# Kernel tuning notes

Hardware: AMD Instinct MI355X
Metric: run time of the kernel (lower is better)

Reference implementation:

```python
import math
import jax, jax.numpy as jnp
import numpy as np

B, S, D, E, K, H = 4, 1024, 768, 8, 2, 2048
NH_ROUTER, NH_COLLAB = 12, 2  # collab heads = min(n_heads, top_k) = 2
EPS = 1e-5


def setup_inputs() -> dict:
    key = jax.random.key(0)
    ks = jax.random.split(key, 16)
    n = lambda k, shp, s=0.02: jax.random.normal(k, shp, jnp.float32) * s
    return {
        "x": jax.random.normal(ks[0], (B, S, D), jnp.float32),
        # parallel expert params (E, D, H) / (E, H, D)
        "w1": n(ks[1], (E, D, H)), "w3": n(ks[2], (E, D, H)), "w2": n(ks[3], (E, H, D)),
        # router self-attention (torch MultiheadAttention packed qkv + out proj)
        "r_in_w": n(ks[4], (3 * D, D)), "r_in_b": jnp.zeros((3 * D,), jnp.float32),
        "r_out_w": n(ks[5], (D, D)), "r_out_b": jnp.zeros((D,), jnp.float32),
        "r_norm_w": jnp.ones((D,), jnp.float32),
        "gate_w": n(ks[6], (E, D)),
        # collaborative cross-attention
        "c_in_w": n(ks[7], (3 * D, D)), "c_in_b": jnp.zeros((3 * D,), jnp.float32),
        "c_out_w": n(ks[8], (D, D)), "c_out_b": jnp.zeros((D,), jnp.float32),
        "c_norm_w": jnp.ones((D,), jnp.float32),
        "ffn_w1": n(ks[9], (D, D)), "ffn_w2": n(ks[10], (D, D)),
        "o_w": n(ks[11], (D, D)),
    }


def _mha(x, in_w, in_b, out_w, out_b, nh):
    # torch nn.MultiheadAttention, batch_first, q=k=v=x; returns out and head-avg probs
    N, L, Dm = x.shape
    hd = Dm // nh
    qkv = x @ in_w.T + in_b                       # (N, L, 3D)
    q, k, v = jnp.split(qkv, 3, axis=-1)
    sp = lambda t: t.reshape(N, L, nh, hd).transpose(0, 2, 1, 3)
    q, k, v = sp(q), sp(k), sp(v)
    probs = jax.nn.softmax(jnp.einsum('nhld,nhmd->nhlm', q, k) / math.sqrt(hd), axis=-1)
    o = jnp.einsum('nhlm,nhmd->nhld', probs, v).transpose(0, 2, 1, 3).reshape(N, L, Dm)
    return o @ out_w.T + out_b, probs.mean(axis=1)


def _rms(x, w):
    return x * jax.lax.rsqrt(jnp.mean(x * x, axis=-1, keepdims=True) + EPS) * w


def reference(x, w1, w3, w2, r_in_w, r_in_b, r_out_w, r_out_b, r_norm_w, gate_w,
              c_in_w, c_in_b, c_out_w, c_out_b, c_norm_w, ffn_w1, ffn_w2, o_w):
    Bx, Sx, Dx = x.shape
    # dense all-expert SwiGLU: (B,S,E,D)
    gate = jnp.einsum('bsd,edh->bseh', x, w1)
    up = jnp.einsum('bsd,edh->bseh', x, w3)
    expert_out = jnp.einsum('bseh,ehd->bsed', jax.nn.silu(gate) * up, w2)
    ef = expert_out.reshape(Bx * Sx, E, Dx)
    # attention-based router over the E experts per token
    ctx, _ = _mha(ef, r_in_w, r_in_b, r_out_w, r_out_b, NH_ROUTER)
    ctx = _rms(ctx + ef, r_norm_w)
    logits = (ctx.mean(axis=1) @ gate_w.T).reshape(Bx, Sx, E)
    routing_probs = jax.nn.softmax(logits, axis=-1)
    tk_logits, tk_idx = jax.lax.top_k(logits, K)  # router_temperature = 1.0
    tk_probs = jax.nn.softmax(tk_logits, axis=-1)
    sel = jnp.take_along_axis(expert_out, tk_idx[..., None], axis=2)  # (B,S,K,D)
    sf = sel.reshape(Bx * Sx, K, Dx)
    # collaborative fusion among selected experts
    ao, aw = _mha(sf, c_in_w, c_in_b, c_out_w, c_out_b, NH_COLLAB)
    ao = _rms(ao + sf, c_norm_w)
    refined = (jax.nn.gelu(ao @ ffn_w1.T, approximate=False) @ ffn_w2.T) + ao
    refined = refined.reshape(Bx, Sx, K, Dx)
    final = jnp.sum(refined * tk_probs[..., None], axis=2) @ o_w.T
    # auxiliary loss
    usage = routing_probs.mean(axis=(0, 1))
    balance = jnp.mean((usage - usage.mean()) ** 2)
    diversity = jnp.mean(-jnp.sum(aw * jnp.log(aw + 1e-9), axis=-1))
    aux = 0.1 * (0.01 * diversity + 0.01 * balance)
    return final, aux, tk_idx
```

## Files before the change

### kernel.cpp

```cpp
#include <hip/hip_runtime.h>


typedef unsigned short u16;
typedef unsigned int u32;
typedef _Float16 f16;
typedef f16 f16x4 __attribute__((ext_vector_type(4)));
typedef f16 f16x8 __attribute__((ext_vector_type(8)));
typedef float f32x4 __attribute__((ext_vector_type(4)));

__device__ __forceinline__ float b2f(u16 v){
  union { u32 u; float f; } x; x.u = ((u32)v) << 16; return x.f;
}
__device__ __forceinline__ u16 f2b(float f){
  union { float f; u32 u; } x; x.f = f;
  u32 u = x.u;
  if ((u & 0x7fffffffu) > 0x7f800000u) return (u16)0x7fc0;
  return (u16)((u + 0x7fffu + ((u >> 16) & 1u)) >> 16);
}
__device__ __forceinline__ float gelu_f(float x){
  return 0.5f * x * (1.f + erff(x * 0.70710678118654752f));
}

template<int NW>
__device__ __forceinline__ float blockReduceSum(float v, float* red){
  #pragma unroll
  for (int o = 32; o > 0; o >>= 1) v += __shfl_down(v, o, 64);
  const int wv = threadIdx.x >> 6, ln = threadIdx.x & 63;
  __syncthreads();
  if (ln == 0) red[wv] = v;
  __syncthreads();
  float s = 0.f;
  #pragma unroll
  for (int i = 0; i < NW; i++) s += red[i];
  return s;
}

__device__ __forceinline__ float waveReduceSum(float v){
  #pragma unroll
  for (int o = 32; o > 0; o >>= 1) v += __shfl_xor(v, o, 64);
  return v;
}

template<int AK, int AOP, bool SPLIT, bool BT, bool BIAS, int ACT, bool RES, bool DUAL, bool SK2>
__global__ __launch_bounds__(256, 2) void mgemm(
    const void* __restrict__ Ap, const float* __restrict__ A2p, int lda, long long strideA,
    const float* __restrict__ B1, const float* __restrict__ B2, int ldb, long long strideB,
    float* __restrict__ C1, float* __restrict__ C2, int ldc, long long strideC,
    const float* __restrict__ bias, const float* __restrict__ resid, int ldr,
    int Kd, int zs)
{
  __shared__ f16 AsH[2][128*40];
  __shared__ f16 BsH[2][128*40];
  __shared__ f16 AsL[SPLIT ? 2 : 1][SPLIT ? 128*40 : 4];
  __shared__ f16 BsL[SPLIT ? 2 : 1][SPLIT ? 128*40 : 4];

  const int tid = threadIdx.x;
  const int m0 = blockIdx.y * 128, n0 = blockIdx.x * 128;
  const int z = blockIdx.z;
  int zi = z, k0 = 0, KL = Kd;
  const float* Bz; float* Cz;
  if constexpr (DUAL){
    if (z < zs){ zi = z;      Bz = B1 + (long long)zi*strideB; Cz = C1 + (long long)zi*strideC; }
    else       { zi = z - zs; Bz = B2 + (long long)zi*strideB; Cz = C2 + (long long)zi*strideC; }
  } else if constexpr (SK2){
    const int s = (z >= zs) ? 1 : 0;
    zi = z - s * zs;
    KL = Kd >> 1; k0 = s * KL;
    Bz = B1 + (long long)zi*strideB + (BT ? (long long)k0 : (long long)k0 * ldb);
    Cz = (s ? C2 : C1) + (long long)zi*strideC;
  } else {
    Bz = B1 + (long long)z*strideB; Cz = C1 + (long long)z*strideC;
  }
  const float* A32  = (const float*)Ap + (AK==0 ? (long long)zi*strideA : 0) + k0;
  const u16*   A16  = (const u16*)Ap   + (AK==1 ? (long long)zi*strideA : 0) + k0;
  const float* A32b = (AOP != 0) ? (A2p + (long long)zi*strideA + k0) : nullptr;

  const int ln = tid & 63, wv = tid >> 6;
  const int wm = (wv >> 1) * 64, wn = (wv & 1) * 64;
  const int fr = ln & 15, fq = ln >> 4;

  const int rA = tid >> 1, kcA = (tid & 1) * 16;
  const int npB = tid & 63, kgB = tid >> 6;

  struct Regs {
    f32x4 av[4]; f32x4 av2[4]; uint4 av16[2]; f32x4 bv[4]; float2 bw[8];
  };
  Regs R0, R1;

  auto loadAB = [&](Regs& R, int kt){
    if constexpr (AK == 0){
      const float* s = A32 + (size_t)(m0 + rA) * lda + kt + kcA;
      #pragma unroll
      for (int j = 0; j < 4; j++) R.av[j] = ((const f32x4*)s)[j];
      if constexpr (AOP != 0){
        const float* s2 = A32b + (size_t)(m0 + rA) * lda + kt + kcA;
        #pragma unroll
        for (int j = 0; j < 4; j++) R.av2[j] = ((const f32x4*)s2)[j];
      }
    } else {
      const u16* s = A16 + (size_t)(m0 + rA) * lda + kt + kcA;
      R.av16[0] = ((const uint4*)s)[0]; R.av16[1] = ((const uint4*)s)[1];
    }
    if constexpr (BT){
      const float* s = Bz + (size_t)(n0 + rA) * ldb + kt + kcA;
      #pragma unroll
      for (int j = 0; j < 4; j++) R.bv[j] = ((const f32x4*)s)[j];
    } else {
      const float* s = Bz + (size_t)(kt + kgB * 8) * ldb + n0 + 2 * npB;
      #pragma unroll
      for (int kk = 0; kk < 8; kk++) R.bw[kk] = *(const float2*)(s + (size_t)kk * ldb);
    }
  };

  auto storeAB = [&](const Regs& R, int b){
    if constexpr (AK == 0){
      #pragma unroll
      for (int jj = 0; jj < 2; jj++){
        f16x8 h, l;
        #pragma unroll
        for (int c = 0; c < 8; c++){
          float v = R.av[jj*2 + (c>>2)][c & 3];
          if constexpr (AOP == 1){
            const float u = R.av2[jj*2 + (c>>2)][c & 3];
            v = (v / (1.f + expf(-v))) * u;
          } else if constexpr (AOP == 2){
            v = v + R.av2[jj*2 + (c>>2)][c & 3];
          } else if constexpr (AOP == 3){
            v = gelu_f(v + R.av2[jj*2 + (c>>2)][c & 3]);
          }
          h[c] = (f16)v;
          if constexpr (SPLIT) l[c] = (f16)(v - (float)h[c]);
        }
        *(f16x8*)&AsH[b][rA*40 + kcA + jj*8] = h;
        if constexpr (SPLIT) *(f16x8*)&AsL[b][rA*40 + kcA + jj*8] = l;
      }
    } else {
      #pragma unroll
      for (int j = 0; j < 2; j++){
        const uint4 v = R.av16[j];
        f16x8 h;
        h[0]=(f16)b2f((u16)(v.x & 0xffff)); h[1]=(f16)b2f((u16)(v.x >> 16));
        h[2]=(f16)b2f((u16)(v.y & 0xffff)); h[3]=(f16)b2f((u16)(v.y >> 16));
        h[4]=(f16)b2f((u16)(v.z & 0xffff)); h[5]=(f16)b2f((u16)(v.z >> 16));
        h[6]=(f16)b2f((u16)(v.w & 0xffff)); h[7]=(f16)b2f((u16)(v.w >> 16));
        *(f16x8*)&AsH[b][rA*40 + kcA + j*8] = h;
      }
    }
    if constexpr (BT){
      #pragma unroll
      for (int jj = 0; jj < 2; jj++){
        f16x8 h, l;
        #pragma unroll
        for (int c = 0; c < 8; c++){
          const float v = R.bv[jj*2 + (c>>2)][c & 3];
          h[c] = (f16)v;
          if constexpr (SPLIT) l[c] = (f16)(v - (float)h[c]);
        }
        *(f16x8*)&BsH[b][rA*40 + kcA + jj*8] = h;
        if constexpr (SPLIT) *(f16x8*)&BsL[b][rA*40 + kcA + jj*8] = l;
      }
    } else {
      #pragma unroll
      for (int c = 0; c < 2; c++){
        const int row = 2*npB + c;
        const int p8 = (kgB + (row >> 3)) & 3;
        f16x8 h, l;
        #pragma unroll
        for (int kk = 0; kk < 8; kk++){
          const float v = c ? R.bw[kk].y : R.bw[kk].x;
          h[kk] = (f16)v;
          if constexpr (SPLIT) l[kk] = (f16)(v - (float)h[kk]);
        }
        *(f16x8*)&BsH[b][row*40 + p8*8] = h;
        if constexpr (SPLIT) *(f16x8*)&BsL[b][row*40 + p8*8] = l;
      }
    }
  };

  f32x4 acc[4][4];
  #pragma unroll
  for (int i = 0; i < 4; i++)
    #pragma unroll
    for (int j = 0; j < 4; j++){ acc[i][j][0]=0.f; acc[i][j][1]=0.f; acc[i][j][2]=0.f; acc[i][j][3]=0.f; }

  int aoff[4], boff[4];
  #pragma unroll
  for (int i = 0; i < 4; i++) aoff[i] = (wm + i*16 + fr)*40 + fq*8;
  #pragma unroll
  for (int j = 0; j < 4; j++){
    const int brow = wn + j*16 + fr;
    boff[j] = brow*40 + (BT ? fq*8 : (((fq + (brow >> 3)) & 3) << 3));
  }

  auto compute = [&](int b){
    f16x8 aH[4], bH[4];
    #pragma unroll
    for (int i = 0; i < 4; i++) aH[i] = *(const f16x8*)&AsH[b][aoff[i]];
    #pragma unroll
    for (int j = 0; j < 4; j++) bH[j] = *(const f16x8*)&BsH[b][boff[j]];
    #pragma unroll
    for (int i = 0; i < 4; i++)
      #pragma unroll
      for (int j = 0; j < 4; j++)
        acc[i][j] = __builtin_amdgcn_mfma_f32_16x16x32_f16(aH[i], bH[j], acc[i][j], 0, 0, 0);
    if constexpr (SPLIT){
      f16x8 aL[4], bL[4];
      #pragma unroll
      for (int i = 0; i < 4; i++) aL[i] = *(const f16x8*)&AsL[b][aoff[i]];
      #pragma unroll
      for (int j = 0; j < 4; j++) bL[j] = *(const f16x8*)&BsL[b][boff[j]];
      #pragma unroll
      for (int i = 0; i < 4; i++)
        #pragma unroll
        for (int j = 0; j < 4; j++){
          acc[i][j] = __builtin_amdgcn_mfma_f32_16x16x32_f16(aH[i], bL[j], acc[i][j], 0, 0, 0);
          acc[i][j] = __builtin_amdgcn_mfma_f32_16x16x32_f16(aL[i], bH[j], acc[i][j], 0, 0, 0);
        }
    }
  };

  const int NT = KL >> 5;
  loadAB(R0, 0);
  loadAB(R1, 32);
  for (int tt = 0; tt < NT; tt += 2){
    storeAB(R0, 0);
    __syncthreads();
    if (tt + 2 < NT) loadAB(R0, (tt + 2) << 5);
    compute(0);
    storeAB(R1, 1);
    __syncthreads();
    if (tt + 3 < NT) loadAB(R1, (tt + 3) << 5);
    compute(1);
  }

  #pragma unroll
  for (int j = 0; j < 4; j++){
    const int n = n0 + wn + j*16 + fr;
    float bvv = 0.f;
    if constexpr (BIAS) bvv = bias[n];
    #pragma unroll
    for (int i = 0; i < 4; i++){
      #pragma unroll
      for (int r = 0; r < 4; r++){
        const int m = m0 + wm + i*16 + fq*4 + r;
        float v = acc[i][j][r];
        if constexpr (BIAS) v += bvv;
        if constexpr (ACT == 1) v = gelu_f(v);
        if constexpr (RES) v += resid[(size_t)m * ldr + n];
        Cz[(size_t)m * ldc + n] = v;
      }
    }
  }
}

__global__ void silu_k(const float4* __restrict__ g, const float4* __restrict__ u,
                       float4* __restrict__ h, int n4){
  const int i = blockIdx.x * 256 + threadIdx.x;
  if (i < n4){
    const float4 gv = g[i], uv = u[i];
    float4 r;
    r.x = (gv.x / (1.f + expf(-gv.x))) * uv.x;
    r.y = (gv.y / (1.f + expf(-gv.y))) * uv.y;
    r.z = (gv.z / (1.f + expf(-gv.z))) * uv.z;
    r.w = (gv.w / (1.f + expf(-gv.w))) * uv.w;
    h[i] = r;
  }
}

template<int ACT, bool RES, bool BIAS>
__global__ void add2_k(float* __restrict__ dst, const float* __restrict__ src,
                       const float* __restrict__ bias, const float* __restrict__ resid,
                       int n4, int ld4){
  const int i = blockIdx.x * 256 + threadIdx.x;
  if (i >= n4) return;
  const f32x4 a = ((const f32x4*)dst)[i];
  const f32x4 b = ((const f32x4*)src)[i];
  const int c4 = (i % ld4) * 4;
  f32x4 r;
  #pragma unroll
  for (int c = 0; c < 4; c++){
    float v = a[c] + b[c];
    if constexpr (BIAS) v += bias[c4 + c];
    if constexpr (ACT == 1) v = gelu_f(v);
    if constexpr (RES) v += resid[(size_t)i * 4 + c];
    r[c] = v;
  }
  ((f32x4*)dst)[i] = r;
}

__global__ __launch_bounds__(128) void router_attn(const float* __restrict__ qkv,
                                                   float* __restrict__ attn_o){
  __shared__ __align__(16) float L[8 * 1536];
  __shared__ float Ps[96][8];
  const int t = blockIdx.x, tid = threadIdx.x;
  const float* src = qkv + (size_t)t * 8 * 2304;
  for (int i = tid; i < 3072; i += 128){
    const int e = i / 384, c4 = i - e * 384;
    ((float4*)L)[i] = ((const float4*)(src + (size_t)e * 2304))[c4];
  }
  __syncthreads();
  if (tid < 96){
    const int h = tid >> 3, e = tid & 7;
    const float* q = L + e * 1536 + h * 64;
    float s[8]; float mx = -1e30f;
    #pragma unroll
    for (int e2 = 0; e2 < 8; e2++){
      const float* kk = L + e2 * 1536 + 768 + h * 64;
      float acc = 0.f;
      #pragma unroll
      for (int d = 0; d < 64; d++) acc = fmaf(q[d], kk[d], acc);
      s[e2] = acc * 0.125f;
      mx = fmaxf(mx, s[e2]);
    }
    float den = 0.f;
    #pragma unroll
    for (int e2 = 0; e2 < 8; e2++){ s[e2] = expf(s[e2] - mx); den += s[e2]; }
    const float inv = 1.f / den;
    #pragma unroll
    for (int e2 = 0; e2 < 8; e2++) Ps[tid][e2] = s[e2] * inv;
  }
  __syncthreads();
  for (int i = tid; i < 1536; i += 128){
    const int e = i / 192, c4 = i - e * 192;
    ((float4*)L)[i] = ((const float4*)(src + (size_t)e * 2304 + 1536))[c4];
  }
  __syncthreads();
  if (tid < 96){
    const int h = tid >> 3, e = tid & 7;
    float p[8];
    #pragma unroll
    for (int e2 = 0; e2 < 8; e2++) p[e2] = Ps[tid][e2];
    float* dst = attn_o + ((size_t)t * 8 + e) * 768 + h * 64;
    for (int d = 0; d < 64; d++){
      float acc = 0.f;
      #pragma unroll
      for (int e2 = 0; e2 < 8; e2++) acc = fmaf(p[e2], L[e2 * 768 + h * 64 + d], acc);
      dst[d] = acc;
    }
  }
}

__global__ __launch_bounds__(256) void router_final(
    const float* __restrict__ proj0, const float* __restrict__ proj1,
    const float* __restrict__ pbias, const float* __restrict__ eoc,
    const float* __restrict__ rnw, const float* __restrict__ gw,
    int t0, float* __restrict__ usage, float* __restrict__ tkp,
    u16* __restrict__ sf, float* __restrict__ oidx)
{
  const int wv = threadIdx.x >> 6, ln = threadIdx.x & 63;
  const int tl = blockIdx.x * 4 + wv, t = t0 + tl;

  float rw[12], pb[12];
  #pragma unroll
  for (int g = 0; g < 3; g++){
    const f32x4 w = ((const f32x4*)rnw)[ln + g * 64];
    const f32x4 bbv = ((const f32x4*)pbias)[ln + g * 64];
    #pragma unroll
    for (int c = 0; c < 4; c++){ rw[g*4 + c] = w[c]; pb[g*4 + c] = bbv[c]; }
  }

  float cs[12];
  #pragma unroll
  for (int i = 0; i < 12; i++) cs[i] = 0.f;

  for (int e = 0; e < 8; e++){
    const size_t ro = ((size_t)tl * 8 + e) * 768;
    float v[12]; float ss = 0.f;
    #pragma unroll
    for (int g = 0; g < 3; g++){
      const f32x4 p0 = ((const f32x4*)(proj0 + ro))[ln + g * 64];
      const f32x4 p1 = ((const f32x4*)(proj1 + ro))[ln + g * 64];
      const f32x4 e0 = ((const f32x4*)(eoc + ro))[ln + g * 64];
      #pragma unroll
      for (int c = 0; c < 4; c++){
        const float vv = ((p0[c] + p1[c]) + pb[g*4 + c]) + e0[c];
        v[g*4 + c] = vv; ss += vv * vv;
      }
    }
    ss = waveReduceSum(ss);
    const float sc = 1.f / sqrtf(ss * (1.f / 768.f) + 1e-5f);
    #pragma unroll
    for (int i = 0; i < 12; i++) cs[i] += v[i] * sc * rw[i];
  }

  float lg[8];
  #pragma unroll
  for (int j = 0; j < 8; j++){
    const float* gwr = gw + j * 768;
    float p = 0.f;
    #pragma unroll
    for (int g = 0; g < 3; g++){
      const f32x4 w = ((const f32x4*)gwr)[ln + g * 64];
      #pragma unroll
      for (int c = 0; c < 4; c++) p += cs[g*4 + c] * w[c];
    }
    lg[j] = waveReduceSum(p) * 0.125f;
  }

  int i0 = 0; float l0 = lg[0];
  #pragma unroll
  for (int j = 1; j < 8; j++) if (lg[j] > l0){ l0 = lg[j]; i0 = j; }
  int i1 = -1; float l1 = -1e30f;
  #pragma unroll
  for (int j = 0; j < 8; j++) if (j != i0 && lg[j] > l1){ l1 = lg[j]; i1 = j; }

  if (ln == 0){
    float mx = -1e30f;
    #pragma unroll
    for (int j = 0; j < 8; j++) mx = fmaxf(mx, lg[j]);
    float ex[8], den = 0.f;
    #pragma unroll
    for (int j = 0; j < 8; j++){ ex[j] = expf(lg[j] - mx); den += ex[j]; }
    const float inv = 1.f / den;
    #pragma unroll
    for (int j = 0; j < 8; j++) atomicAdd(&usage[j], ex[j] * inv);
    const float e1v = expf(l1 - l0);
    const float p0 = 1.f / (1.f + e1v);
    tkp[(size_t)t * 2]     = p0;
    tkp[(size_t)t * 2 + 1] = e1v * p0;
    oidx[(size_t)t * 2]     = (float)i0;
    oidx[(size_t)t * 2 + 1] = (float)i1;
  }

  #pragma unroll
  for (int s = 0; s < 2; s++){
    const int ie = s ? i1 : i0;
    const size_t ro = ((size_t)tl * 8 + ie) * 768;
    #pragma unroll
    for (int g = 0; g < 3; g++){
      const f32x4 a = ((const f32x4*)(eoc + ro))[ln + g * 64];
      ushort4 o;
      o.x = f2b(a[0]); o.y = f2b(a[1]); o.z = f2b(a[2]); o.w = f2b(a[3]);
      *(ushort4*)&sf[((size_t)t * 2 + s) * 768 + 4 * (ln + g * 64)] = o;
    }
  }
}

__global__ __launch_bounds__(128) void collab_attn(
    const float* __restrict__ qkv, float* __restrict__ attn_o, float* __restrict__ divsum)
{
  const int t = blockIdx.x, tid = threadIdx.x;
  __shared__ __align__(16) float L[4608];
  __shared__ float P[8];
  __shared__ float red[2];
  const float* src = qkv + (size_t)t * 4608;
  for (int i = tid; i < 1152; i += 128) ((float4*)L)[i] = ((const float4*)src)[i];
  __syncthreads();
  for (int hij = 0; hij < 8; hij++){
    const int h = hij >> 2, qi = (hij >> 1) & 1, kj = hij & 1;
    const float* q = L + qi * 2304 + h * 384;
    const float* k = L + kj * 2304 + 768 + h * 384;
    float acc = 0.f;
    for (int d = tid; d < 384; d += 128) acc += q[d] * k[d];
    acc = blockReduceSum<2>(acc, red);
    if (tid == 0) P[hij] = acc;
  }
  __syncthreads();
  if (tid == 0){
    const float scale = 0.051031036307982884f;
    float aw[2][2] = {{0.f,0.f},{0.f,0.f}};
    for (int h = 0; h < 2; h++)
      for (int i = 0; i < 2; i++){
        const float s0 = P[h*4 + i*2 + 0] * scale, s1 = P[h*4 + i*2 + 1] * scale;
        const float m = fmaxf(s0, s1);
        const float e0 = expf(s0 - m), e1 = expf(s1 - m), inv = 1.f / (e0 + e1);
        P[h*4 + i*2 + 0] = e0 * inv; P[h*4 + i*2 + 1] = e1 * inv;
        aw[i][0] += 0.5f * e0 * inv; aw[i][1] += 0.5f * e1 * inv;
      }
    float ent = 0.f;
    for (int i = 0; i < 2; i++)
      for (int j = 0; j < 2; j++) ent -= aw[i][j] * logf(aw[i][j] + 1e-9f);
    atomicAdd(divsum, ent);
  }
  __syncthreads();
  for (int c = tid; c < 768; c += 128){
    const int h = c / 384;
    const float v0 = L[1536 + c], v1 = L[3840 + c];
    attn_o[((size_t)t * 2 + 0) * 768 + c] = P[h*4 + 0] * v0 + P[h*4 + 1] * v1;
    attn_o[((size_t)t * 2 + 1) * 768 + c] = P[h*4 + 2] * v0 + P[h*4 + 3] * v1;
  }
}

__global__ __launch_bounds__(256) void rms2_k(
    const float* __restrict__ a0, const float* __restrict__ a1,
    const float* __restrict__ bb, const u16* __restrict__ rb,
    const float* __restrict__ wt, float* __restrict__ o){
  const int r = blockIdx.x, tid = threadIdx.x;
  __shared__ float red[4];
  float v[3]; float ss = 0.f;
  #pragma unroll
  for (int i = 0; i < 3; i++){
    const int c = tid + i * 256;
    const float t = (a0[(size_t)r * 768 + c] + a1[(size_t)r * 768 + c]) + bb[c];
    v[i] = t + b2f(rb[(size_t)r * 768 + c]);
    ss += v[i] * v[i];
  }
  ss = blockReduceSum<4>(ss, red);
  const float sc = 1.f / sqrtf(ss * (1.f / 768.f) + 1e-5f);
  #pragma unroll
  for (int i = 0; i < 3; i++){
    const int c = tid + i * 256;
    o[(size_t)r * 768 + c] = v[i] * sc * wt[c];
  }
}

__global__ void wsum3(const float* __restrict__ pA, const float* __restrict__ pB,
                      const float* __restrict__ ao, const float* __restrict__ tkp,
                      float* __restrict__ y){
  const int idx = blockIdx.x * 256 + threadIdx.x;
  const int t = idx / 768, c = idx - t * 768;
  const size_t r0 = ((size_t)t * 2) * 768 + c, r1 = r0 + 768;
  const float v0 = (pA[r0] + pB[r0]) + ao[r0];
  const float v1 = (pA[r1] + pB[r1]) + ao[r1];
  y[idx] = tkp[t * 2] * v0 + tkp[t * 2 + 1] * v1;
}

__global__ void aux_k(const float* __restrict__ usage, const float* __restrict__ divsum,
                      float* __restrict__ out){
  if (threadIdx.x == 0 && blockIdx.x == 0){
    float u[8], s = 0.f;
    for (int e = 0; e < 8; e++){ u[e] = usage[e] * (1.f / 4096.f); s += u[e]; }
    const float mean = s * 0.125f;
    float bal = 0.f;
    for (int e = 0; e < 8; e++){ const float d = u[e] - mean; bal += d * d; }
    bal *= 0.125f;
    const float div = divsum[0] * (1.f / 8192.f);
    out[0] = 0.1f * (0.01f * div + 0.01f * bal);
  }
}

__global__ void zero_k(float* p, int n){
  const int i = blockIdx.x * 64 + threadIdx.x;
  if (i < n) p[i] = 0.f;
}

extern "C" void kernel_launch(void* const* d_in, const int* in_sizes, int n_in,
                              void* d_out, int out_size, void* d_ws, size_t ws_size,
                              hipStream_t stream)
{
  (void)in_sizes; (void)n_in; (void)out_size; (void)ws_size;
  const float* x       = (const float*)d_in[0];
  const float* w1      = (const float*)d_in[1];
  const float* w3      = (const float*)d_in[2];
  const float* w2      = (const float*)d_in[3];
  const float* r_in_w  = (const float*)d_in[4];
  const float* r_in_b  = (const float*)d_in[5];
  const float* r_out_w = (const float*)d_in[6];
  const float* r_out_b = (const float*)d_in[7];
  const float* r_norm_w= (const float*)d_in[8];
  const float* gate_w  = (const float*)d_in[9];
  const float* c_in_w  = (const float*)d_in[10];
  const float* c_in_b  = (const float*)d_in[11];
  const float* c_out_w = (const float*)d_in[12];
  const float* c_out_b = (const float*)d_in[13];
  const float* c_norm_w= (const float*)d_in[14];
  const float* ffn_w1  = (const float*)d_in[15];
  const float* ffn_w2  = (const float*)d_in[16];
  const float* o_w     = (const float*)d_in[17];

  char* wsb   = (char*)d_ws;
  char* arena = wsb;
  float* eoc  = (float*)(wsb + 33554432);
  u16*   sf   = (u16*)  (wsb + 39845888);
  float* tkp  = (float*)(wsb + 52428800);
  float* usage= (float*)(wsb + 52461568);

  float* gateb = (float*)(arena);
  float* upb   = (float*)(arena + 16777216);
  float* qkvr  = (float*)(arena);
  float* aor   = (float*)(arena + 18874368);
  float* projr = (float*)(arena + 25165824);
  float* pr2   = (float*)(arena);

  float* qkvc  = (float*)(arena);
  float* aoc   = (float*)(arena + 18874368);
  float* pc1   = (float*)(arena + 25165824);
  float* pc2   = (float*)(arena);
  float* aob   = (float*)(arena + 6291456);
  float* pf1   = (float*)(arena + 12582912);
  float* pf2   = (float*)(arena + 18874368);
  float* ybuf  = (float*)(arena + 12582912);
  float* fo2   = (float*)(arena + 18874368);

  float* outp    = (float*)d_out;
  float* out_aux = outp + (size_t)4096*768;
  float* out_idx = out_aux + 1;

  zero_k<<<1, 64, 0, stream>>>(usage, 16);

  for (int cch = 0; cch < 16; cch++){
    const int t0 = cch * 256;
    mgemm<0,0,true,false,false,0,false,true,false><<<dim3(16,2,16),256,0,stream>>>(
      x + (size_t)t0*768, nullptr, 768, 0LL,
      w1, w3, 2048, 1572864LL,
      gateb, upb, 2048, 524288LL,
      nullptr, nullptr, 0, 768, 8);
    silu_k<<<4096, 256, 0, stream>>>((const float4*)gateb, (const float4*)upb,
                                     (float4*)gateb, 1048576);
    mgemm<0,0,true,false,false,0,false,false,true><<<dim3(6,2,16),256,0,stream>>>(
      gateb, nullptr, 2048, 524288LL,
      w2, nullptr, 768, 1572864LL,
      eoc, upb, 6144, 768LL,
      nullptr, nullptr, 0, 2048, 8);
    add2_k<0,false,false><<<1536, 256, 0, stream>>>(eoc, upb, nullptr, nullptr, 393216, 192);
    mgemm<0,0,true,true,true,0,false,false,false><<<dim3(18,16,1),256,0,stream>>>(
      eoc, nullptr, 768, 0LL, r_in_w, nullptr, 768, 0LL,
      qkvr, nullptr, 2304, 0LL, r_in_b, nullptr, 0, 768, 0);
    router_attn<<<256, 128, 0, stream>>>(qkvr, aor);
    mgemm<0,0,true,true,false,0,false,false,true><<<dim3(6,16,2),256,0,stream>>>(
      aor, nullptr, 768, 0LL, r_out_w, nullptr, 768, 0LL,
      projr, pr2, 768, 0LL, nullptr, nullptr, 0, 768, 1);
    router_final<<<64, 256, 0, stream>>>(projr, pr2, r_out_b, eoc,
                                         r_norm_w, gate_w, t0, usage, tkp, sf, out_idx);
  }

  for (int q = 0; q < 4; q++){
    const int tq0 = q * 1024;
    const u16* sf_q = sf + (size_t)tq0 * 2 * 768;
    mgemm<1,0,false,true,true,0,false,false,false><<<dim3(18,16,1),256,0,stream>>>(
      sf_q, nullptr, 768, 0LL, c_in_w, nullptr, 768, 0LL,
      qkvc, nullptr, 2304, 0LL, c_in_b, nullptr, 0, 768, 0);
    collab_attn<<<1024, 128, 0, stream>>>(qkvc, aoc, usage + 8);
    mgemm<0,0,false,true,false,0,false,false,true><<<dim3(6,16,2),256,0,stream>>>(
      aoc, nullptr, 768, 0LL, c_out_w, nullptr, 768, 0LL,
      pc1, pc2, 768, 0LL, nullptr, nullptr, 0, 768, 1);
    rms2_k<<<2048, 256, 0, stream>>>(pc1, pc2, c_out_b, sf_q, c_norm_w, aob);
    mgemm<0,0,false,true,false,0,false,false,true><<<dim3(6,16,2),256,0,stream>>>(
      aob, nullptr, 768, 0LL, ffn_w1, nullptr, 768, 0LL,
      pf1, pf2, 768, 0LL, nullptr, nullptr, 0, 768, 1);
    mgemm<0,3,false,true,false,0,false,false,true><<<dim3(6,16,2),256,0,stream>>>(
      pf1, pf2, 768, 0LL, ffn_w2, nullptr, 768, 0LL,
      pc1, pc2, 768, 0LL, nullptr, nullptr, 0, 768, 1);
    wsum3<<<3072, 256, 0, stream>>>(pc1, pc2, aob, tkp + (size_t)tq0 * 2, ybuf);
    mgemm<0,0,false,true,false,0,false,false,true><<<dim3(6,8,2),256,0,stream>>>(
      ybuf, nullptr, 768, 0LL, o_w, nullptr, 768, 0LL,
      outp + (size_t)tq0 * 768, fo2, 768, 0LL, nullptr, nullptr, 0, 768, 1);
    add2_k<0,false,false><<<768, 256, 0, stream>>>(outp + (size_t)tq0 * 768, fo2,
                                                   nullptr, nullptr, 196608, 192);
  }
  aux_k<<<1, 64, 0, stream>>>(usage, usage + 8, out_aux);
}
```

Before: 4.444 ms.

## Use nontemporal loads/stores for streaming intermediates and simplify GEMM prefetch to single register set

Adds an NTC template flag so GEMM epilogues write results with nontemporal stores, and switches the elementwise, attention and reduction kernels to nontemporal loads and stores on intermediate buffers that are read once. This aims to keep the large streamed intermediates from evicting reused weights in cache. The GEMM main loop also drops the two-register-set prefetch for a single set loaded one tile ahead, and unused AOP fusion branches are removed. This lowers register pressure but shortens the prefetch distance, and nontemporal stores can hurt when the next kernel rereads the data right away.

```diff
diff --git a/kernel.cpp b/kernel.cpp
--- a/kernel.cpp
+++ b/kernel.cpp
@@ -41,7 +41,7 @@
   return v;
 }
 
-template<int AK, int AOP, bool SPLIT, bool BT, bool BIAS, int ACT, bool RES, bool DUAL, bool SK2>
+template<int AK, int AOP, bool SPLIT, bool BT, bool BIAS, int ACT, bool RES, bool DUAL, bool SK2, bool NTC>
 __global__ __launch_bounds__(256, 2) void mgemm(
     const void* __restrict__ Ap, const float* __restrict__ A2p, int lda, long long strideA,
     const float* __restrict__ B1, const float* __restrict__ B2, int ldb, long long strideB,
@@ -82,51 +82,43 @@
   const int rA = tid >> 1, kcA = (tid & 1) * 16;
   const int npB = tid & 63, kgB = tid >> 6;
 
-  struct Regs {
-    f32x4 av[4]; f32x4 av2[4]; uint4 av16[2]; f32x4 bv[4]; float2 bw[8];
-  };
-  Regs R0, R1;
-
-  auto loadAB = [&](Regs& R, int kt){
+  f32x4 av[4]; f32x4 av2[4]; uint4 av16[2]; f32x4 bv[4]; float2 bw[8];
+
+  auto loadAB = [&](int kt){
     if constexpr (AK == 0){
       const float* s = A32 + (size_t)(m0 + rA) * lda + kt + kcA;
       #pragma unroll
-      for (int j = 0; j < 4; j++) R.av[j] = ((const f32x4*)s)[j];
+      for (int j = 0; j < 4; j++) av[j] = ((const f32x4*)s)[j];
       if constexpr (AOP != 0){
         const float* s2 = A32b + (size_t)(m0 + rA) * lda + kt + kcA;
         #pragma unroll
-        for (int j = 0; j < 4; j++) R.av2[j] = ((const f32x4*)s2)[j];
+        for (int j = 0; j < 4; j++) av2[j] = ((const f32x4*)s2)[j];
       }
     } else {
       const u16* s = A16 + (size_t)(m0 + rA) * lda + kt + kcA;
-      R.av16[0] = ((const uint4*)s)[0]; R.av16[1] = ((const uint4*)s)[1];
+      av16[0] = ((const uint4*)s)[0]; av16[1] = ((const uint4*)s)[1];
     }
     if constexpr (BT){
       const float* s = Bz + (size_t)(n0 + rA) * ldb + kt + kcA;
       #pragma unroll
-      for (int j = 0; j < 4; j++) R.bv[j] = ((const f32x4*)s)[j];
+      for (int j = 0; j < 4; j++) bv[j] = ((const f32x4*)s)[j];
     } else {
       const float* s = Bz + (size_t)(kt + kgB * 8) * ldb + n0 + 2 * npB;
       #pragma unroll
-      for (int kk = 0; kk < 8; kk++) R.bw[kk] = *(const float2*)(s + (size_t)kk * ldb);
+      for (int kk = 0; kk < 8; kk++) bw[kk] = *(const float2*)(s + (size_t)kk * ldb);
     }
   };
 
-  auto storeAB = [&](const Regs& R, int b){
+  auto storeAB = [&](int b){
     if constexpr (AK == 0){
       #pragma unroll
       for (int jj = 0; jj < 2; jj++){
         f16x8 h, l;
         #pragma unroll
         for (int c = 0; c < 8; c++){
-          float v = R.av[jj*2 + (c>>2)][c & 3];
-          if constexpr (AOP == 1){
-            const float u = R.av2[jj*2 + (c>>2)][c & 3];
-            v = (v / (1.f + expf(-v))) * u;
-          } else if constexpr (AOP == 2){
-            v = v + R.av2[jj*2 + (c>>2)][c & 3];
-          } else if constexpr (AOP == 3){
-            v = gelu_f(v + R.av2[jj*2 + (c>>2)][c & 3]);
+          float v = av[jj*2 + (c>>2)][c & 3];
+          if constexpr (AOP == 3){
+            v = gelu_f(v + av2[jj*2 + (c>>2)][c & 3]);
           }
           h[c] = (f16)v;
           if constexpr (SPLIT) l[c] = (f16)(v - (float)h[c]);
@@ -137,7 +129,7 @@
     } else {
       #pragma unroll
       for (int j = 0; j < 2; j++){
-        const uint4 v = R.av16[j];
+        const uint4 v = av16[j];
         f16x8 h;
         h[0]=(f16)b2f((u16)(v.x & 0xffff)); h[1]=(f16)b2f((u16)(v.x >> 16));
         h[2]=(f16)b2f((u16)(v.y & 0xffff)); h[3]=(f16)b2f((u16)(v.y >> 16));
@@ -152,7 +144,7 @@
         f16x8 h, l;
         #pragma unroll
         for (int c = 0; c < 8; c++){
-          const float v = R.bv[jj*2 + (c>>2)][c & 3];
+          const float v = bv[jj*2 + (c>>2)][c & 3];
           h[c] = (f16)v;
           if constexpr (SPLIT) l[c] = (f16)(v - (float)h[c]);
         }
@@ -167,7 +159,7 @@
         f16x8 h, l;
         #pragma unroll
         for (int kk = 0; kk < 8; kk++){
-          const float v = c ? R.bw[kk].y : R.bw[kk].x;
+          const float v = c ? bw[kk].y : bw[kk].x;
           h[kk] = (f16)v;
           if constexpr (SPLIT) l[kk] = (f16)(v - (float)h[kk]);
         }
@@ -192,7 +184,13 @@
     boff[j] = brow*40 + (BT ? fq*8 : (((fq + (brow >> 3)) & 3) << 3));
   }
 
-  auto compute = [&](int b){
+  loadAB(0);
+  const int NT = KL >> 5;
+  for (int t = 0; t < NT; t++){
+    const int b = t & 1;
+    storeAB(b);
+    __syncthreads();
+    if (t + 1 < NT) loadAB((t + 1) << 5);
     f16x8 aH[4], bH[4];
     #pragma unroll
     for (int i = 0; i < 4; i++) aH[i] = *(const f16x8*)&AsH[b][aoff[i]];
@@ -217,20 +215,6 @@
           acc[i][j] = __builtin_amdgcn_mfma_f32_16x16x32_f16(aL[i], bH[j], acc[i][j], 0, 0, 0);
         }
     }
-  };
-
-  const int NT = KL >> 5;
-  loadAB(R0, 0);
-  loadAB(R1, 32);
-  for (int tt = 0; tt < NT; tt += 2){
-    storeAB(R0, 0);
-    __syncthreads();
-    if (tt + 2 < NT) loadAB(R0, (tt + 2) << 5);
-    compute(0);
-    storeAB(R1, 1);
-    __syncthreads();
-    if (tt + 3 < NT) loadAB(R1, (tt + 3) << 5);
-    compute(1);
   }
 
   #pragma unroll
@@ -247,23 +231,24 @@
         if constexpr (BIAS) v += bvv;
         if constexpr (ACT == 1) v = gelu_f(v);
         if constexpr (RES) v += resid[(size_t)m * ldr + n];
-        Cz[(size_t)m * ldc + n] = v;
-      }
-    }
-  }
-}
-
-__global__ void silu_k(const float4* __restrict__ g, const float4* __restrict__ u,
-                       float4* __restrict__ h, int n4){
+        if constexpr (NTC) __builtin_nontemporal_store(v, &Cz[(size_t)m * ldc + n]);
+        else               Cz[(size_t)m * ldc + n] = v;
+      }
+    }
+  }
+}
+
+__global__ void silu_k(const f32x4* __restrict__ g, const f32x4* __restrict__ u,
+                       f32x4* __restrict__ h, int n4){
   const int i = blockIdx.x * 256 + threadIdx.x;
   if (i < n4){
-    const float4 gv = g[i], uv = u[i];
-    float4 r;
-    r.x = (gv.x / (1.f + expf(-gv.x))) * uv.x;
-    r.y = (gv.y / (1.f + expf(-gv.y))) * uv.y;
-    r.z = (gv.z / (1.f + expf(-gv.z))) * uv.z;
-    r.w = (gv.w / (1.f + expf(-gv.w))) * uv.w;
-    h[i] = r;
+    const f32x4 gv = __builtin_nontemporal_load(&g[i]);
+    const f32x4 uv = __builtin_nontemporal_load(&u[i]);
+    f32x4 r;
+    #pragma unroll
+    for (int c = 0; c < 4; c++)
+      r[c] = (gv[c] / (1.f + expf(-gv[c]))) * uv[c];
+    __builtin_nontemporal_store(r, &h[i]);
   }
 }
 
@@ -273,8 +258,8 @@
                        int n4, int ld4){
   const int i = blockIdx.x * 256 + threadIdx.x;
   if (i >= n4) return;
-  const f32x4 a = ((const f32x4*)dst)[i];
-  const f32x4 b = ((const f32x4*)src)[i];
+  const f32x4 a = __builtin_nontemporal_load(&((const f32x4*)dst)[i]);
+  const f32x4 b = __builtin_nontemporal_load(&((const f32x4*)src)[i]);
   const int c4 = (i % ld4) * 4;
   f32x4 r;
   #pragma unroll
@@ -285,7 +270,7 @@
     if constexpr (RES) v += resid[(size_t)i * 4 + c];
     r[c] = v;
   }
-  ((f32x4*)dst)[i] = r;
+  __builtin_nontemporal_store(r, &((f32x4*)dst)[i]);
 }
 
 __global__ __launch_bounds__(128) void router_attn(const float* __restrict__ qkv,
@@ -296,7 +281,7 @@
   const float* src = qkv + (size_t)t * 8 * 2304;
   for (int i = tid; i < 3072; i += 128){
     const int e = i / 384, c4 = i - e * 384;
-    ((float4*)L)[i] = ((const float4*)(src + (size_t)e * 2304))[c4];
+    ((f32x4*)L)[i] = __builtin_nontemporal_load(&((const f32x4*)(src + (size_t)e * 2304))[c4]);
   }
   __syncthreads();
   if (tid < 96){
@@ -322,7 +307,7 @@
   __syncthreads();
   for (int i = tid; i < 1536; i += 128){
     const int e = i / 192, c4 = i - e * 192;
-    ((float4*)L)[i] = ((const float4*)(src + (size_t)e * 2304 + 1536))[c4];
+    ((f32x4*)L)[i] = __builtin_nontemporal_load(&((const f32x4*)(src + (size_t)e * 2304 + 1536))[c4]);
   }
   __syncthreads();
   if (tid < 96){
@@ -368,8 +353,8 @@
     float v[12]; float ss = 0.f;
     #pragma unroll
     for (int g = 0; g < 3; g++){
-      const f32x4 p0 = ((const f32x4*)(proj0 + ro))[ln + g * 64];
-      const f32x4 p1 = ((const f32x4*)(proj1 + ro))[ln + g * 64];
+      const f32x4 p0 = __builtin_nontemporal_load(&((const f32x4*)(proj0 + ro))[ln + g * 64]);
+      const f32x4 p1 = __builtin_nontemporal_load(&((const f32x4*)(proj1 + ro))[ln + g * 64]);
       const f32x4 e0 = ((const f32x4*)(eoc + ro))[ln + g * 64];
       #pragma unroll
       for (int c = 0; c < 4; c++){
@@ -444,7 +429,8 @@
   __shared__ float P[8];
   __shared__ float red[2];
   const float* src = qkv + (size_t)t * 4608;
-  for (int i = tid; i < 1152; i += 128) ((float4*)L)[i] = ((const float4*)src)[i];
+  for (int i = tid; i < 1152; i += 128)
+    ((f32x4*)L)[i] = __builtin_nontemporal_load(&((const f32x4*)src)[i]);
   __syncthreads();
   for (int hij = 0; hij < 8; hij++){
     const int h = hij >> 2, qi = (hij >> 1) & 1, kj = hij & 1;
@@ -491,7 +477,8 @@
   #pragma unroll
   for (int i = 0; i < 3; i++){
     const int c = tid + i * 256;
-    const float t = (a0[(size_t)r * 768 + c] + a1[(size_t)r * 768 + c]) + bb[c];
+    const float t = (__builtin_nontemporal_load(&a0[(size_t)r * 768 + c])
+                   + __builtin_nontemporal_load(&a1[(size_t)r * 768 + c])) + bb[c];
     v[i] = t + b2f(rb[(size_t)r * 768 + c]);
     ss += v[i] * v[i];
   }
@@ -510,8 +497,8 @@
   const int idx = blockIdx.x * 256 + threadIdx.x;
   const int t = idx / 768, c = idx - t * 768;
   const size_t r0 = ((size_t)t * 2) * 768 + c, r1 = r0 + 768;
-  const float v0 = (pA[r0] + pB[r0]) + ao[r0];
-  const float v1 = (pA[r1] + pB[r1]) + ao[r1];
+  const float v0 = (__builtin_nontemporal_load(&pA[r0]) + __builtin_nontemporal_load(&pB[r0])) + ao[r0];
+  const float v1 = (__builtin_nontemporal_load(&pA[r1]) + __builtin_nontemporal_load(&pB[r1])) + ao[r1];
   y[idx] = tkp[t * 2] * v0 + tkp[t * 2 + 1] * v1;
 }
 
@@ -590,24 +577,24 @@
 
   for (int cch = 0; cch < 16; cch++){
     const int t0 = cch * 256;
-    mgemm<0,0,true,false,false,0,false,true,false><<<dim3(16,2,16),256,0,stream>>>(
+    mgemm<0,0,true,false,false,0,false,true,false,true><<<dim3(16,2,16),256,0,stream>>>(
       x + (size_t)t0*768, nullptr, 768, 0LL,
       w1, w3, 2048, 1572864LL,
       gateb, upb, 2048, 524288LL,
       nullptr, nullptr, 0, 768, 8);
-    silu_k<<<4096, 256, 0, stream>>>((const float4*)gateb, (const float4*)upb,
-                                     (float4*)gateb, 1048576);
-    mgemm<0,0,true,false,false,0,false,false,true><<<dim3(6,2,16),256,0,stream>>>(
+    silu_k<<<4096, 256, 0, stream>>>((const f32x4*)gateb, (const f32x4*)upb,
+                                     (f32x4*)gateb, 1048576);
+    mgemm<0,0,true,false,false,0,false,false,true,true><<<dim3(6,2,16),256,0,stream>>>(
       gateb, nullptr, 2048, 524288LL,
       w2, nullptr, 768, 1572864LL,
       eoc, upb, 6144, 768LL,
       nullptr, nullptr, 0, 2048, 8);
     add2_k<0,false,false><<<1536, 256, 0, stream>>>(eoc, upb, nullptr, nullptr, 393216, 192);
-    mgemm<0,0,true,true,true,0,false,false,false><<<dim3(18,16,1),256,0,stream>>>(
+    mgemm<0,0,true,true,true,0,false,false,false,true><<<dim3(18,16,1),256,0,stream>>>(
       eoc, nullptr, 768, 0LL, r_in_w, nullptr, 768, 0LL,
       qkvr, nullptr, 2304, 0LL, r_in_b, nullptr, 0, 768, 0);
     router_attn<<<256, 128, 0, stream>>>(qkvr, aor);
-    mgemm<0,0,true,true,false,0,false,false,true><<<dim3(6,16,2),256,0,stream>>>(
+    mgemm<0,0,true,true,false,0,false,false,true,true><<<dim3(6,16,2),256,0,stream>>>(
       aor, nullptr, 768, 0LL, r_out_w, nullptr, 768, 0LL,
       projr, pr2, 768, 0LL, nullptr, nullptr, 0, 768, 1);
     router_final<<<64, 256, 0, stream>>>(projr, pr2, r_out_b, eoc,
@@ -617,22 +604,22 @@
   for (int q = 0; q < 4; q++){
     const int tq0 = q * 1024;
     const u16* sf_q = sf + (size_t)tq0 * 2 * 768;
-    mgemm<1,0,false,true,true,0,false,false,false><<<dim3(18,16,1),256,0,stream>>>(
+    mgemm<1,0,false,true,true,0,false,false,false,true><<<dim3(18,16,1),256,0,stream>>>(
       sf_q, nullptr, 768, 0LL, c_in_w, nullptr, 768, 0LL,
       qkvc, nullptr, 2304, 0LL, c_in_b, nullptr, 0, 768, 0);
     collab_attn<<<1024, 128, 0, stream>>>(qkvc, aoc, usage + 8);
-    mgemm<0,0,false,true,false,0,false,false,true><<<dim3(6,16,2),256,0,stream>>>(
+    mgemm<0,0,false,true,false,0,false,false,true,true><<<dim3(6,16,2),256,0,stream>>>(
       aoc, nullptr, 768, 0LL, c_out_w, nullptr, 768, 0LL,
       pc1, pc2, 768, 0LL, nullptr, nullptr, 0, 768, 1);
     rms2_k<<<2048, 256, 0, stream>>>(pc1, pc2, c_out_b, sf_q, c_norm_w, aob);
-    mgemm<0,0,false,true,false,0,false,false,true><<<dim3(6,16,2),256,0,stream>>>(
+    mgemm<0,0,false,true,false,0,false,false,true,true><<<dim3(6,16,2),256,0,stream>>>(
       aob, nullptr, 768, 0LL, ffn_w1, nullptr, 768, 0LL,
       pf1, pf2, 768, 0LL, nullptr, nullptr, 0, 768, 1);
-    mgemm<0,3,false,true,false,0,false,false,true><<<dim3(6,16,2),256,0,stream>>>(
+    mgemm<0,3,false,true,false,0,false,false,true,true><<<dim3(6,16,2),256,0,stream>>>(
       pf1, pf2, 768, 0LL, ffn_w2, nullptr, 768, 0LL,
       pc1, pc2, 768, 0LL, nullptr, nullptr, 0, 768, 1);
     wsum3<<<3072, 256, 0, stream>>>(pc1, pc2, aob, tkp + (size_t)tq0 * 2, ybuf);
-    mgemm<0,0,false,true,false,0,false,false,true><<<dim3(6,8,2),256,0,stream>>>(
+    mgemm<0,0,false,true,false,0,false,false,true,true><<<dim3(6,8,2),256,0,stream>>>(
       ybuf, nullptr, 768, 0LL, o_w, nullptr, 768, 0LL,
       outp + (size_t)tq0 * 768, fo2, 768, 0LL, nullptr, nullptr, 0, 768, 1);
     add2_k<0,false,false><<<768, 256, 0, stream>>>(outp + (size_t)tq0 * 768, fo2,
```

After: 4.560 ms. +2.6%, slower.
